# Optimization experiments

Hardware: AMD Instinct MI355X
Metric: run time of the kernel (lower is better)

Reference implementation:

```python
import jax, jax.numpy as jnp
import numpy as np

N_NODES = 524288
N_EDGES = 786432
NUM_GRAPHS = 8192
NUM_NODE_TYPES = 16
NODE_DIM = 256
EDGE_DIM = 128
OUT_DIM = 1


def setup_inputs() -> dict:
    key = jax.random.key(0)
    ks = jax.random.split(key, 12)
    h_node = jax.random.uniform(ks[0], (N_NODES, NUM_NODE_TYPES), dtype=jnp.float32)
    pos_node = jax.random.normal(ks[1], (N_NODES, 3), dtype=jnp.float32)
    batch_node = jnp.sort(jax.random.randint(ks[2], (N_NODES,), 0, NUM_GRAPHS)).astype(jnp.int64)
    edge_index = jax.random.randint(ks[3], (2, N_EDGES), 0, N_NODES).astype(jnp.int64)
    batch_edge = jnp.sort(jax.random.randint(ks[4], (N_EDGES,), 0, NUM_GRAPHS)).astype(jnp.int64)
    s = 0.05
    W_node = jax.random.normal(ks[5], (NUM_NODE_TYPES, NODE_DIM), dtype=jnp.float32) * s
    W_edge = jax.random.normal(ks[6], (2 * NUM_NODE_TYPES, EDGE_DIM), dtype=jnp.float32) * s
    H = NODE_DIM + EDGE_DIM
    W1 = jax.random.normal(ks[7], (H, H), dtype=jnp.float32) * s
    b1 = jnp.zeros((H,), dtype=jnp.float32)
    W2 = jax.random.normal(ks[8], (H, OUT_DIM), dtype=jnp.float32) * s
    b2 = jnp.zeros((OUT_DIM,), dtype=jnp.float32)
    return {"h_node": h_node, "pos_node": pos_node, "batch_node": batch_node,
            "edge_index": edge_index, "batch_edge": batch_edge,
            "W_node": W_node, "W_edge": W_edge, "W1": W1, "b1": b1, "W2": W2, "b2": b2}


def _segment_mean(x, seg_ids, num_segments):
    # fused replacement for the original per-graph boolean-mask loop:
    # h[seg==k].mean(0) for all k, via one scatter-add + count normalize
    sums = jax.ops.segment_sum(x, seg_ids, num_segments=num_segments)
    cnts = jax.ops.segment_sum(jnp.ones((x.shape[0],), x.dtype), seg_ids, num_segments=num_segments)
    return sums / jnp.maximum(cnts, 1.0)[:, None]


def reference(h_node, pos_node, batch_node, edge_index, batch_edge,
              W_node, W_edge, W1, b1, W2, b2):
    # h_edge = cat(h_node[src], h_node[dst])  -> [E, 2*num_node_types]
    h_edge_raw = jnp.concatenate([h_node[edge_index[0]], h_node[edge_index[1]]], axis=-1)
    # num_timesteps == 0 path: plain embedders, no time embedding
    hn = h_node @ W_node          # [N, node_dim]
    he = h_edge_raw @ W_edge      # [E, edge_dim]
    # encoder treated as identity (NodeEdgeNet not in scope); pooling is the target op
    node_mean = _segment_mean(hn, batch_node, NUM_GRAPHS)  # [G, node_dim]
    edge_mean = _segment_mean(he, batch_edge, NUM_GRAPHS)  # [G, edge_dim]
    h_sub = jnp.concatenate([node_mean, edge_mean], axis=-1)  # [G, node_dim+edge_dim]
    # final MLP (num_layer=2): Linear -> ReLU -> Linear
    pred = jax.nn.relu(h_sub @ W1 + b1) @ W2 + b2  # [G, 1]
    return pred
```

## Files before the change

kernel.cpp:

```cpp
#include <hip/hip_runtime.h>

#define N_NODES_C   524288
#define N_EDGES_C   786432
#define NUM_GRAPHS_C 8192
#define NT 16
#define NODE_DIM_C 256
#define EDGE_DIM_C 128
#define HDIM 384
#define KC 48

#define FOLD_BLOCKS  72
#define EDGE_BLOCKS  2048
#define NODE_BLOCKS  2048
#define EDGE_BASE    FOLD_BLOCKS
#define NODE_BASE    (FOLD_BLOCKS + EDGE_BLOCKS)
#define TOTAL_BLOCKS (FOLD_BLOCKS + EDGE_BLOCKS + NODE_BLOCKS)

#define WS_NM    0
#define WS_EM    524288
#define WS_WC    1572864

__device__ __forceinline__ int lower_bound_i32(const int* __restrict__ a, int n, int key) {
    int lo = 0, hi = n;
    while (lo < hi) {
        int mid = (lo + hi) >> 1;
        if (a[mid] < key) lo = mid + 1; else hi = mid;
    }
    return lo;
}

__device__ __forceinline__ void wave_seg_bounds(const int* __restrict__ b, int n,
                                                int g, int lane, int& s, int& e) {
    int key = g + ((lane >= 32) ? 1 : 0);
    int lo = lower_bound_i32(b, n, key);
    s = __shfl(lo, 0, 64);
    e = __shfl(lo, 32, 64);
}

__device__ __forceinline__ void f4_add(float4& a, const float4 v) {
    a.x += v.x; a.y += v.y; a.z += v.z; a.w += v.w;
}

__device__ __forceinline__ void f4_shfl_xor_add(float4& a, int mask) {
    a.x += __shfl_xor(a.x, mask, 64);
    a.y += __shfl_xor(a.y, mask, 64);
    a.z += __shfl_xor(a.z, mask, 64);
    a.w += __shfl_xor(a.w, mask, 64);
}

__global__ __launch_bounds__(256) void km_mega(
    const float* __restrict__ h_node,
    const int* __restrict__ bnode, const int* __restrict__ bedge,
    const int* __restrict__ esrc, const int* __restrict__ edst,
    const float* __restrict__ Wn, const float* __restrict__ We,
    const float* __restrict__ W1,
    float* __restrict__ nm, float* __restrict__ em, float* __restrict__ Wc) {
    int blk  = blockIdx.x;
    int wave = threadIdx.x >> 6;
    int lane = threadIdx.x & 63;
    const float4* h4 = (const float4*)h_node;

    if (blk < FOLD_BLOCKS) {
        int o = blk * 256 + threadIdx.x;
        if (o >= KC * HDIM) return;
        int k = o / HDIM, j = o % HDIM;
        float acc = 0.f;
        if (k < NT) {
            const float* wr = &Wn[k * NODE_DIM_C];
            #pragma unroll 16
            for (int kk = 0; kk < NODE_DIM_C; ++kk)
                acc = fmaf(wr[kk], W1[(size_t)kk * HDIM + j], acc);
        } else {
            const float* wr = &We[(k - NT) * EDGE_DIM_C];
            #pragma unroll 16
            for (int kk = 0; kk < EDGE_DIM_C; ++kk)
                acc = fmaf(wr[kk], W1[(size_t)(NODE_DIM_C + kk) * HDIM + j], acc);
        }
        Wc[o] = acc;
    } else if (blk < NODE_BASE) {
        int g = (blk - EDGE_BASE) * 4 + wave;
        int s, e;
        wave_seg_bounds(bedge, N_EDGES_C, g, lane, s, e);
        int eo   = lane >> 3;
        int p    = (lane >> 2) & 1;
        int quad = lane & 3;
        const int* __restrict__ idxp = p ? edst : esrc;
        float4 accA = make_float4(0.f, 0.f, 0.f, 0.f);
        float4 accB = accA;
        int iA = s + eo, iB = s + eo + 8;
        int nxA = (iA < e) ? idxp[iA] : -1;
        int nxB = (iB < e) ? idxp[iB] : -1;
        while (nxB >= 0) {
            int idxA = nxA, idxB = nxB;
            iA += 16; iB += 16;
            nxA = (iA < e) ? idxp[iA] : -1;
            nxB = (iB < e) ? idxp[iB] : -1;
            float4 va = h4[(size_t)idxA * 4 + quad];
            float4 vb = h4[(size_t)idxB * 4 + quad];
            accA.x += va.x; accA.y += va.y; accA.z += va.z; accA.w += va.w;
            accB.x += vb.x; accB.y += vb.y; accB.z += vb.z; accB.w += vb.w;
        }
        if (nxA >= 0) {
            float4 v = h4[(size_t)nxA * 4 + quad];
            accA.x += v.x; accA.y += v.y; accA.z += v.z; accA.w += v.w;
        }
        accA.x += accB.x; accA.y += accB.y; accA.z += accB.z; accA.w += accB.w;
        f4_shfl_xor_add(accA, 8);
        f4_shfl_xor_add(accA, 16);
        f4_shfl_xor_add(accA, 32);
        if (eo == 0) {
            float inv = 1.f / fmaxf((float)(e - s), 1.f);
            ((float4*)em)[(size_t)g * 8 + p * 4 + quad] =
                make_float4(accA.x * inv, accA.y * inv, accA.z * inv, accA.w * inv);
        }
    } else {
        int g = (blk - NODE_BASE) * 4 + wave;
        int s, e;
        wave_seg_bounds(bnode, N_NODES_C, g, lane, s, e);
        int row_off = lane >> 2;
        int quad    = lane & 3;
        float4 a0 = make_float4(0.f, 0.f, 0.f, 0.f);
        float4 a1 = a0;
        int i = s + row_off;
        for (; i + 16 < e; i += 32) {
            float4 v0 = h4[(size_t)i * 4 + quad];
            float4 v1 = h4[(size_t)(i + 16) * 4 + quad];
            f4_add(a0, v0);
            f4_add(a1, v1);
        }
        if (i < e) f4_add(a0, h4[(size_t)i * 4 + quad]);
        f4_add(a0, a1);
        f4_shfl_xor_add(a0, 4);
        f4_shfl_xor_add(a0, 8);
        f4_shfl_xor_add(a0, 16);
        f4_shfl_xor_add(a0, 32);
        if (row_off == 0) {
            float inv = 1.f / fmaxf((float)(e - s), 1.f);
            ((float4*)nm)[(size_t)g * 4 + quad] =
                make_float4(a0.x * inv, a0.y * inv, a0.z * inv, a0.w * inv);
        }
    }
}

#define GPB 16
__global__ __launch_bounds__(HDIM) void k3_mlp(
    const float* __restrict__ nm, const float* __restrict__ em,
    const float* __restrict__ Wc, const float* __restrict__ b1,
    const float* __restrict__ W2, const float* __restrict__ b2,
    float* __restrict__ pred) {
    int j = threadIdx.x;
    float wc[KC];
    #pragma unroll
    for (int k = 0; k < KC; ++k) wc[k] = Wc[k * HDIM + j];
    float b1j = b1[j], w2j = W2[j], b20 = b2[0];

    __shared__ float fs[GPB][KC];
    __shared__ float part[GPB][6];
    int g0 = blockIdx.x * GPB;
    #pragma unroll
    for (int t = j; t < GPB * KC; t += HDIM) {
        int g = t / KC, k = t % KC;
        fs[g][k] = (k < NT) ? nm[(size_t)(g0 + g) * NT + k]
                            : em[(size_t)(g0 + g) * 32 + (k - NT)];
    }
    __syncthreads();

    int wave = j >> 6, lane = j & 63;
    for (int g = 0; g < GPB; ++g) {
        float z = b1j;
        #pragma unroll
        for (int k = 0; k < KC; ++k) z = fmaf(fs[g][k], wc[k], z);
        z = fmaxf(z, 0.f);
        float p = z * w2j;
        #pragma unroll
        for (int off = 32; off > 0; off >>= 1) p += __shfl_down(p, off, 64);
        if (lane == 0) part[g][wave] = p;
    }
    __syncthreads();
    if (j < GPB) {
        float sacc = b20;
        #pragma unroll
        for (int w = 0; w < 6; ++w) sacc += part[j][w];
        pred[g0 + j] = sacc;
    }
}

extern "C" void kernel_launch(void* const* d_in, const int* in_sizes, int n_in,
                              void* d_out, int out_size, void* d_ws, size_t ws_size,
                              hipStream_t stream) {
    const float* h_node     = (const float*)d_in[0];
    const int*   batch_node = (const int*)d_in[2];
    const int*   edge_index = (const int*)d_in[3];
    const int*   batch_edge = (const int*)d_in[4];
    const float* W_node     = (const float*)d_in[5];
    const float* W_edge     = (const float*)d_in[6];
    const float* W1         = (const float*)d_in[7];
    const float* b1         = (const float*)d_in[8];
    const float* W2         = (const float*)d_in[9];
    const float* b2         = (const float*)d_in[10];
    float* pred = (float*)d_out;

    char* ws = (char*)d_ws;
    float* nm = (float*)(ws + WS_NM);
    float* em = (float*)(ws + WS_EM);
    float* Wc = (float*)(ws + WS_WC);

    const int* esrc = edge_index;
    const int* edst = edge_index + N_EDGES_C;

    km_mega<<<TOTAL_BLOCKS, 256, 0, stream>>>(
        h_node, batch_node, batch_edge, esrc, edst, W_node, W_edge, W1, nm, em, Wc);
    k3_mlp<<<NUM_GRAPHS_C / GPB, HDIM, 0, stream>>>(nm, em, Wc, b1, W2, b2, pred);
}
```

Baseline: 147.7 us.

## Interleave edge/node blocks and software-pipeline edge gather with four accumulators

Block scheduling changes so that edge-gather and node-reduction blocks alternate in groups of eight, with the weight-fold blocks moved to the end of the grid, which mixes latency-bound gather work with streaming work on each CU. The edge loop is rewritten to keep four independent rows in flight per lane, loading indices two iterations ahead and row data one iteration ahead. The goal is to hide the dependent index-then-row gather latency. The cost is higher register pressure and some extra predicated loads.

```diff
diff --git a/kernel.cpp b/kernel.cpp
--- a/kernel.cpp
+++ b/kernel.cpp
@@ -9,12 +9,10 @@
 #define HDIM 384
 #define KC 48
 
+#define PAIR_BLOCKS  4096
 #define FOLD_BLOCKS  72
-#define EDGE_BLOCKS  2048
-#define NODE_BLOCKS  2048
-#define EDGE_BASE    FOLD_BLOCKS
-#define NODE_BASE    (FOLD_BLOCKS + EDGE_BLOCKS)
-#define TOTAL_BLOCKS (FOLD_BLOCKS + EDGE_BLOCKS + NODE_BLOCKS)
+#define FOLD_BASE    PAIR_BLOCKS
+#define TOTAL_BLOCKS (PAIR_BLOCKS + FOLD_BLOCKS)
 
 #define WS_NM    0
 #define WS_EM    524288
@@ -60,8 +58,8 @@
     int lane = threadIdx.x & 63;
     const float4* h4 = (const float4*)h_node;
 
-    if (blk < FOLD_BLOCKS) {
-        int o = blk * 256 + threadIdx.x;
+    if (blk >= FOLD_BASE) {
+        int o = (blk - FOLD_BASE) * 256 + threadIdx.x;
         if (o >= KC * HDIM) return;
         int k = o / HDIM, j = o % HDIM;
         float acc = 0.f;
@@ -77,44 +75,65 @@
                 acc = fmaf(wr[kk], W1[(size_t)(NODE_DIM_C + kk) * HDIM + j], acc);
         }
         Wc[o] = acc;
-    } else if (blk < NODE_BASE) {
-        int g = (blk - EDGE_BASE) * 4 + wave;
+        return;
+    }
+
+    int role = (blk >> 3) & 1;
+    int v    = ((blk >> 4) << 3) | (blk & 7);
+    int g    = v * 4 + wave;
+
+    if (role == 0) {
         int s, e;
         wave_seg_bounds(bedge, N_EDGES_C, g, lane, s, e);
         int eo   = lane >> 3;
         int p    = (lane >> 2) & 1;
         int quad = lane & 3;
         const int* __restrict__ idxp = p ? edst : esrc;
-        float4 accA = make_float4(0.f, 0.f, 0.f, 0.f);
-        float4 accB = accA;
-        int iA = s + eo, iB = s + eo + 8;
-        int nxA = (iA < e) ? idxp[iA] : -1;
-        int nxB = (iB < e) ? idxp[iB] : -1;
-        while (nxB >= 0) {
-            int idxA = nxA, idxB = nxB;
-            iA += 16; iB += 16;
-            nxA = (iA < e) ? idxp[iA] : -1;
-            nxB = (iB < e) ? idxp[iB] : -1;
-            float4 va = h4[(size_t)idxA * 4 + quad];
-            float4 vb = h4[(size_t)idxB * 4 + quad];
-            accA.x += va.x; accA.y += va.y; accA.z += va.z; accA.w += va.w;
-            accB.x += vb.x; accB.y += vb.y; accB.z += vb.z; accB.w += vb.w;
-        }
-        if (nxA >= 0) {
-            float4 v = h4[(size_t)nxA * 4 + quad];
-            accA.x += v.x; accA.y += v.y; accA.z += v.z; accA.w += v.w;
-        }
-        accA.x += accB.x; accA.y += accB.y; accA.z += accB.z; accA.w += accB.w;
-        f4_shfl_xor_add(accA, 8);
-        f4_shfl_xor_add(accA, 16);
-        f4_shfl_xor_add(accA, 32);
+        const float4 z4 = make_float4(0.f, 0.f, 0.f, 0.f);
+        float4 a0 = z4, a1 = z4, a2 = z4, a3 = z4;
+
+        int cnt = e - s;
+        int T = (cnt + 31) >> 5;
+        int j0 = s + eo, j1 = j0 + 8, j2 = j0 + 16, j3 = j0 + 24;
+
+        int n0 = (j0 < e) ? idxp[j0] : -1;
+        int n1 = (j1 < e) ? idxp[j1] : -1;
+        int n2 = (j2 < e) ? idxp[j2] : -1;
+        int n3 = (j3 < e) ? idxp[j3] : -1;
+        int m0 = (j0 + 32 < e) ? idxp[j0 + 32] : -1;
+        int m1 = (j1 + 32 < e) ? idxp[j1 + 32] : -1;
+        int m2 = (j2 + 32 < e) ? idxp[j2 + 32] : -1;
+        int m3 = (j3 + 32 < e) ? idxp[j3 + 32] : -1;
+        float4 v0 = (n0 >= 0) ? h4[(size_t)n0 * 4 + quad] : z4;
+        float4 v1 = (n1 >= 0) ? h4[(size_t)n1 * 4 + quad] : z4;
+        float4 v2 = (n2 >= 0) ? h4[(size_t)n2 * 4 + quad] : z4;
+        float4 v3 = (n3 >= 0) ? h4[(size_t)n3 * 4 + quad] : z4;
+
+        for (int t = 1; t < T; ++t) {
+            j0 += 32; j1 += 32; j2 += 32; j3 += 32;
+            int q0 = (j0 + 32 < e) ? idxp[j0 + 32] : -1;
+            int q1 = (j1 + 32 < e) ? idxp[j1 + 32] : -1;
+            int q2 = (j2 + 32 < e) ? idxp[j2 + 32] : -1;
+            int q3 = (j3 + 32 < e) ? idxp[j3 + 32] : -1;
+            float4 w0 = (m0 >= 0) ? h4[(size_t)m0 * 4 + quad] : z4;
+            float4 w1 = (m1 >= 0) ? h4[(size_t)m1 * 4 + quad] : z4;
+            float4 w2 = (m2 >= 0) ? h4[(size_t)m2 * 4 + quad] : z4;
+            float4 w3 = (m3 >= 0) ? h4[(size_t)m3 * 4 + quad] : z4;
+            f4_add(a0, v0); f4_add(a1, v1); f4_add(a2, v2); f4_add(a3, v3);
+            v0 = w0; v1 = w1; v2 = w2; v3 = w3;
+            m0 = q0; m1 = q1; m2 = q2; m3 = q3;
+        }
+        f4_add(a0, v0); f4_add(a1, v1); f4_add(a2, v2); f4_add(a3, v3);
+        f4_add(a0, a1); f4_add(a2, a3); f4_add(a0, a2);
+        f4_shfl_xor_add(a0, 8);
+        f4_shfl_xor_add(a0, 16);
+        f4_shfl_xor_add(a0, 32);
         if (eo == 0) {
-            float inv = 1.f / fmaxf((float)(e - s), 1.f);
+            float inv = 1.f / fmaxf((float)cnt, 1.f);
             ((float4*)em)[(size_t)g * 8 + p * 4 + quad] =
-                make_float4(accA.x * inv, accA.y * inv, accA.z * inv, accA.w * inv);
+                make_float4(a0.x * inv, a0.y * inv, a0.z * inv, a0.w * inv);
         }
     } else {
-        int g = (blk - NODE_BASE) * 4 + wave;
         int s, e;
         wave_seg_bounds(bnode, N_NODES_C, g, lane, s, e);
         int row_off = lane >> 2;
```

New measurement: 153.6 us. 1.04x slower.

## Precompute segment offsets and slice edge gathers by node range with atomics

Applied to the files above, without the earlier changes.

A new prep kernel builds per-graph start offsets for nodes and edges from the sorted batch arrays and zeroes the edge-mean buffer. This replaces the per-wave binary searches. The edge pooling is split into 8 slices by source/destination node index range, so each block only gathers h_node rows from a 64K-node window, aiming for better L2 locality. Partial means are combined with float atomics. The cost is an extra launch, 8x redundant index reads, atomic traffic, and non-deterministic summation order.

```diff
diff --git a/kernel.cpp b/kernel.cpp
--- a/kernel.cpp
+++ b/kernel.cpp
@@ -10,32 +10,18 @@
 #define KC 48
 
 #define FOLD_BLOCKS  72
-#define EDGE_BLOCKS  2048
+#define EDGE_BLOCKS  16384
 #define NODE_BLOCKS  2048
 #define EDGE_BASE    FOLD_BLOCKS
 #define NODE_BASE    (FOLD_BLOCKS + EDGE_BLOCKS)
 #define TOTAL_BLOCKS (FOLD_BLOCKS + EDGE_BLOCKS + NODE_BLOCKS)
+#define K0_BLOCKS    3072
 
 #define WS_NM    0
 #define WS_EM    524288
 #define WS_WC    1572864
-
-__device__ __forceinline__ int lower_bound_i32(const int* __restrict__ a, int n, int key) {
-    int lo = 0, hi = n;
-    while (lo < hi) {
-        int mid = (lo + hi) >> 1;
-        if (a[mid] < key) lo = mid + 1; else hi = mid;
-    }
-    return lo;
-}
-
-__device__ __forceinline__ void wave_seg_bounds(const int* __restrict__ b, int n,
-                                                int g, int lane, int& s, int& e) {
-    int key = g + ((lane >= 32) ? 1 : 0);
-    int lo = lower_bound_i32(b, n, key);
-    s = __shfl(lo, 0, 64);
-    e = __shfl(lo, 32, 64);
-}
+#define WS_ES    1646592
+#define WS_NS    1679364
 
 __device__ __forceinline__ void f4_add(float4& a, const float4 v) {
     a.x += v.x; a.y += v.y; a.z += v.z; a.w += v.w;
@@ -48,10 +34,29 @@
     a.w += __shfl_xor(a.w, mask, 64);
 }
 
+__global__ __launch_bounds__(256) void k0_prep(
+    const int* __restrict__ bnode, const int* __restrict__ bedge,
+    int* __restrict__ estart, int* __restrict__ nstart, float* __restrict__ em) {
+    int i = blockIdx.x * 256 + threadIdx.x;
+    if (i < NUM_GRAPHS_C * 32) em[i] = 0.f;
+    if (i < N_EDGES_C) {
+        int g0 = bedge[i];
+        int hi = (i + 1 < N_EDGES_C) ? bedge[i + 1] : NUM_GRAPHS_C;
+        if (i == 0) for (int g = 0; g <= g0; ++g) estart[g] = 0;
+        for (int g = g0 + 1; g <= hi; ++g) estart[g] = i + 1;
+    }
+    if (i < N_NODES_C) {
+        int g0 = bnode[i];
+        int hi = (i + 1 < N_NODES_C) ? bnode[i + 1] : NUM_GRAPHS_C;
+        if (i == 0) for (int g = 0; g <= g0; ++g) nstart[g] = 0;
+        for (int g = g0 + 1; g <= hi; ++g) nstart[g] = i + 1;
+    }
+}
+
 __global__ __launch_bounds__(256) void km_mega(
     const float* __restrict__ h_node,
-    const int* __restrict__ bnode, const int* __restrict__ bedge,
     const int* __restrict__ esrc, const int* __restrict__ edst,
+    const int* __restrict__ estart, const int* __restrict__ nstart,
     const float* __restrict__ Wn, const float* __restrict__ We,
     const float* __restrict__ W1,
     float* __restrict__ nm, float* __restrict__ em, float* __restrict__ Wc) {
@@ -59,6 +64,7 @@
     int wave = threadIdx.x >> 6;
     int lane = threadIdx.x & 63;
     const float4* h4 = (const float4*)h_node;
+    const float4 z4 = make_float4(0.f, 0.f, 0.f, 0.f);
 
     if (blk < FOLD_BLOCKS) {
         int o = blk * 256 + threadIdx.x;
@@ -78,16 +84,16 @@
         }
         Wc[o] = acc;
     } else if (blk < NODE_BASE) {
-        int g = (blk - EDGE_BASE) * 4 + wave;
-        int s, e;
-        wave_seg_bounds(bedge, N_EDGES_C, g, lane, s, e);
+        int eb    = blk - EDGE_BASE;
+        int slice = eb & 7;
+        int g     = (eb >> 3) * 4 + wave;
+        int s = estart[g], e = estart[g + 1];
         int eo   = lane >> 3;
         int p    = (lane >> 2) & 1;
         int quad = lane & 3;
         const int* __restrict__ idxp = p ? edst : esrc;
-        float4 accA = make_float4(0.f, 0.f, 0.f, 0.f);
-        float4 accB = accA;
-        int iA = s + eo, iB = s + eo + 8;
+        float4 accA = z4, accB = z4;
+        int iA = s + eo, iB = iA + 8;
         int nxA = (iA < e) ? idxp[iA] : -1;
         int nxB = (iB < e) ? idxp[iB] : -1;
         while (nxB >= 0) {
@@ -95,32 +101,29 @@
             iA += 16; iB += 16;
             nxA = (iA < e) ? idxp[iA] : -1;
             nxB = (iB < e) ? idxp[iB] : -1;
-            float4 va = h4[(size_t)idxA * 4 + quad];
-            float4 vb = h4[(size_t)idxB * 4 + quad];
-            accA.x += va.x; accA.y += va.y; accA.z += va.z; accA.w += va.w;
-            accB.x += vb.x; accB.y += vb.y; accB.z += vb.z; accB.w += vb.w;
-        }
-        if (nxA >= 0) {
-            float4 v = h4[(size_t)nxA * 4 + quad];
-            accA.x += v.x; accA.y += v.y; accA.z += v.z; accA.w += v.w;
-        }
-        accA.x += accB.x; accA.y += accB.y; accA.z += accB.z; accA.w += accB.w;
+            if ((idxA >> 16) == slice) f4_add(accA, h4[(size_t)idxA * 4 + quad]);
+            if ((idxB >> 16) == slice) f4_add(accB, h4[(size_t)idxB * 4 + quad]);
+        }
+        if (nxA >= 0 && (nxA >> 16) == slice)
+            f4_add(accA, h4[(size_t)nxA * 4 + quad]);
+        f4_add(accA, accB);
         f4_shfl_xor_add(accA, 8);
         f4_shfl_xor_add(accA, 16);
         f4_shfl_xor_add(accA, 32);
         if (eo == 0) {
             float inv = 1.f / fmaxf((float)(e - s), 1.f);
-            ((float4*)em)[(size_t)g * 8 + p * 4 + quad] =
-                make_float4(accA.x * inv, accA.y * inv, accA.z * inv, accA.w * inv);
+            float* dst = &em[(size_t)g * 32 + p * 16 + quad * 4];
+            atomicAdd(dst + 0, accA.x * inv);
+            atomicAdd(dst + 1, accA.y * inv);
+            atomicAdd(dst + 2, accA.z * inv);
+            atomicAdd(dst + 3, accA.w * inv);
         }
     } else {
         int g = (blk - NODE_BASE) * 4 + wave;
-        int s, e;
-        wave_seg_bounds(bnode, N_NODES_C, g, lane, s, e);
+        int s = nstart[g], e = nstart[g + 1];
         int row_off = lane >> 2;
         int quad    = lane & 3;
-        float4 a0 = make_float4(0.f, 0.f, 0.f, 0.f);
-        float4 a1 = a0;
+        float4 a0 = z4, a1 = z4;
         int i = s + row_off;
         for (; i + 16 < e; i += 32) {
             float4 v0 = h4[(size_t)i * 4 + quad];
@@ -201,14 +204,17 @@
     float* pred = (float*)d_out;
 
     char* ws = (char*)d_ws;
-    float* nm = (float*)(ws + WS_NM);
-    float* em = (float*)(ws + WS_EM);
-    float* Wc = (float*)(ws + WS_WC);
+    float* nm     = (float*)(ws + WS_NM);
+    float* em     = (float*)(ws + WS_EM);
+    float* Wc     = (float*)(ws + WS_WC);
+    int*   estart = (int*)(ws + WS_ES);
+    int*   nstart = (int*)(ws + WS_NS);
 
     const int* esrc = edge_index;
     const int* edst = edge_index + N_EDGES_C;
 
+    k0_prep<<<K0_BLOCKS, 256, 0, stream>>>(batch_node, batch_edge, estart, nstart, em);
     km_mega<<<TOTAL_BLOCKS, 256, 0, stream>>>(
-        h_node, batch_node, batch_edge, esrc, edst, W_node, W_edge, W1, nm, em, Wc);
+        h_node, esrc, edst, estart, nstart, W_node, W_edge, W1, nm, em, Wc);
     k3_mlp<<<NUM_GRAPHS_C / GPB, HDIM, 0, stream>>>(nm, em, Wc, b1, W2, b2, pred);
 }
```

New measurement: 174.5 us. +18.1%, slower.
